# Kernel tuning notes

Hardware: AMD Instinct MI355X
Metric: run time of the kernel (lower is better)

## Reference

```python
import jax, jax.numpy as jnp
import numpy as np

N = 20000      # number of nodes
K = 32         # neighbors per node (per edge type)
D_FEAT = 128   # feature dim


def setup_inputs() -> dict:
    key = jax.random.key(0)
    k1, k2, k3 = jax.random.split(key, 3)
    feat = jax.random.normal(k1, (N, D_FEAT), dtype=jnp.float32)
    sim_idx = jax.random.randint(k2, (N, K), 0, N)
    cor_idx = jax.random.randint(k3, (N, K), 0, N)
    return {"feat": feat, "sim_idx": sim_idx, "cor_idx": cor_idx}


def _coattention(Dm, Qm):
    # Dm, Qm: [N, K, d]
    L = jnp.einsum('nkd,njd->nkj', Dm, Qm)          # [N, K, K]
    AC = jax.nn.softmax(L, axis=-1)                  # softmax over Q-neighbors
    AS = jax.nn.softmax(jnp.swapaxes(L, 1, 2), axis=-1)  # softmax over D-neighbors
    CQ = jnp.einsum('nkj,njd->nkd', AC, Qm)          # [N, K, d]
    CD = jnp.einsum('nkj,njd->nkd', AS, jnp.concatenate([Dm, CQ], axis=-1))  # [N, K, 2d]
    return jnp.concatenate([Qm, CD], axis=-1)        # [N, K, 3d]


def reference(feat, sim_idx, cor_idx):
    # mode == 'cor': D <- sim edges, Q <- cor edges (dropout=0 => identity)
    Dm = feat[sim_idx]   # [N, K, d] gather
    Qm = feat[cor_idx]   # [N, K, d] gather
    h = _coattention(Dm, Qm)                          # [N, K, 3d]
    n, k, td = h.shape
    # AvgPool1d(kernel=3, stride=3) over last dim -> [N, K, d]
    h = h.reshape(n, k, td // 3, 3).mean(axis=-1)
    h_neigh = h.mean(axis=1)                          # mean over K neighbors -> [N, d]
    return feat + h_neigh
```

## Files before the change

### kernel.cpp

```cpp
#include <hip/hip_runtime.h>

#define KN 32
#define DF 128
#define WPB 2

typedef float  f32x16 __attribute__((ext_vector_type(16)));
typedef float  f32x2  __attribute__((ext_vector_type(2)));
typedef short  s16x8  __attribute__((ext_vector_type(8)));

union ldsu { int4 i; s16x8 v; };

__device__ __forceinline__ unsigned int pk_bf16(float lo, float hi) {
    unsigned int r;
    asm("v_cvt_pk_bf16_f32 %0, %1, %2" : "=v"(r) : "v"(lo), "v"(hi));
    return r;
}

__global__ __launch_bounds__(256)
void cvt_kernel(const float* __restrict__ f, unsigned short* __restrict__ bf,
                unsigned char* __restrict__ f8, int n8) {
    const int i = blockIdx.x * blockDim.x + threadIdx.x;
    if (i >= n8) return;
    float4 x0 = ((const float4*)f)[2 * i];
    float4 x1 = ((const float4*)f)[2 * i + 1];
    int4 b;
    b.x = (int)pk_bf16(x0.x, x0.y); b.y = (int)pk_bf16(x0.z, x0.w);
    b.z = (int)pk_bf16(x1.x, x1.y); b.w = (int)pk_bf16(x1.z, x1.w);
    ((int4*)bf)[i] = b;
    int p0 = __builtin_amdgcn_cvt_pk_fp8_f32(x0.x, x0.y, 0, false);
    p0     = __builtin_amdgcn_cvt_pk_fp8_f32(x0.z, x0.w, p0, true);
    int p1 = __builtin_amdgcn_cvt_pk_fp8_f32(x1.x, x1.y, 0, false);
    p1     = __builtin_amdgcn_cvt_pk_fp8_f32(x1.z, x1.w, p1, true);
    ((int2*)f8)[i] = make_int2(p0, p1);
}

__global__ __launch_bounds__(WPB * 64, 2)
void coattn_kernel(const float* __restrict__ feat,
                   const unsigned char* __restrict__ featbf,
                   const unsigned char* __restrict__ feat8,
                   const int* __restrict__ sim_idx,
                   const int* __restrict__ cor_idx,
                   float* __restrict__ out, int nnodes) {
    __shared__ int4 Ls[WPB][2][KN][8];
    const int wv = threadIdx.x >> 6;
    const int l  = threadIdx.x & 63;
    const int c  = l & 31;
    const int h  = l >> 5;
    const int g  = l >> 3;
    const int m  = l & 7;
    const int n  = blockIdx.x * WPB + wv;
    if (n >= nnodes) return;

    const int si = sim_idx[n * KN + c];
    const int ci = cor_idx[n * KN + c];

    int4 (* const LsD)[8] = Ls[wv][0];
    int4 (* const LsQ)[8] = Ls[wv][1];

    f32x16 acc  = {0,0,0,0,0,0,0,0,0,0,0,0,0,0,0,0};
    f32x16 accT = {0,0,0,0,0,0,0,0,0,0,0,0,0,0,0,0};
    #pragma unroll
    for (int H = 0; H < 2; ++H) {
        int4 gD[4], gQ[4];
        #pragma unroll
        for (int t = 0; t < 4; ++t) {
            const unsigned rD = (unsigned)__shfl(si, 8 * t + g, 64);
            const unsigned rQ = (unsigned)__shfl(ci, 8 * t + g, 64);
            const unsigned off = (unsigned)(H * 128 + m * 16);
            gD[t] = *(const int4*)(featbf + rD * 256u + off);
            gQ[t] = *(const int4*)(featbf + rQ * 256u + off);
        }
        if (H == 1) {
            asm volatile("s_waitcnt lgkmcnt(0)" ::: "memory");
            __builtin_amdgcn_sched_barrier(0);
        }
        #pragma unroll
        for (int t = 0; t < 4; ++t) {
            LsD[8 * t + g][m ^ g] = gD[t];
            LsQ[8 * t + g][m ^ g] = gQ[t];
        }
        asm volatile("s_waitcnt lgkmcnt(0)" ::: "memory");
        __builtin_amdgcn_sched_barrier(0);
        #pragma unroll
        for (int sp = 0; sp < 4; ++sp) {
            union ldsu uD, uQ;
            uD.i = LsD[c][(sp * 2 + h) ^ (c & 7)];
            uQ.i = LsQ[c][(sp * 2 + h) ^ (c & 7)];
            acc  = __builtin_amdgcn_mfma_f32_32x32x16_bf16(uD.v, uQ.v, acc,  0, 0, 0);
            accT = __builtin_amdgcn_mfma_f32_32x32x16_bf16(uQ.v, uD.v, accT, 0, 0, 0);
        }
    }

    float mx = acc[0];
    #pragma unroll
    for (int p = 1; p < 16; ++p) mx = fmaxf(mx, acc[p]);
    mx = fmaxf(mx, __shfl_xor(mx, 32, 64));
    float z = 0.f;
    #pragma unroll
    for (int p = 0; p < 16; ++p) z += __expf(acc[p] - mx);
    z += __shfl_xor(z, 32, 64);
    const float invZ = 1.0f / z;

    float rm = accT[0];
    #pragma unroll
    for (int p = 1; p < 16; ++p) rm = fmaxf(rm, accT[p]);
    rm = fmaxf(rm, __shfl_xor(rm, 32, 64));
    float rs = 0.f;
    #pragma unroll
    for (int p = 0; p < 16; ++p) rs += __expf(accT[p] - rm);
    rs += __shfl_xor(rs, 32, 64);
    const float invR = 1.0f / rs;

    float w = 0.f;
    #pragma unroll
    for (int p = 0; p < 16; ++p) {
        const int jp = (p & 3) + 8 * (p >> 2) + 4 * h;
        w += __expf(accT[p] - __shfl(mx, jp, 64)) * __shfl(invZ, jp, 64);
    }
    w += __shfl_xor(w, 32, 64);

    const float u = w * invR;
    float v = 0.f;
    #pragma unroll
    for (int p = 0; p < 16; ++p) {
        const int kp = (p & 3) + 8 * (p >> 2) + 4 * h;
        v += __expf(acc[p] - __shfl(rm, kp, 64)) * __shfl(u, kp, 64);
    }
    v += __shfl_xor(v, 32, 64);

    float sQ[4] = {0,0,0,0}, sD[4] = {0,0,0,0}, sC[4] = {0,0,0,0};
    #pragma unroll
    for (int t = 0; t < 16; ++t) {
        const int b = h * 16 + t;
        const unsigned rD = (unsigned)__shfl(si, b, 64);
        const unsigned rQ = (unsigned)__shfl(ci, b, 64);
        const float wb = __shfl(w, b, 64);
        const float vb = __shfl(v, b, 64);
        const unsigned int da = *(const unsigned int*)(feat8 + (rD << 7) + 4u * c);
        const unsigned int dq = *(const unsigned int*)(feat8 + (rQ << 7) + 4u * c);
        f32x2 a01 = __builtin_amdgcn_cvt_pk_f32_fp8((int)da, false);
        f32x2 a23 = __builtin_amdgcn_cvt_pk_f32_fp8((int)da, true);
        f32x2 q01 = __builtin_amdgcn_cvt_pk_f32_fp8((int)dq, false);
        f32x2 q23 = __builtin_amdgcn_cvt_pk_f32_fp8((int)dq, true);
        sQ[0] += q01[0]; sQ[1] += q01[1]; sQ[2] += q23[0]; sQ[3] += q23[1];
        sD[0] = fmaf(wb, a01[0], sD[0]); sD[1] = fmaf(wb, a01[1], sD[1]);
        sD[2] = fmaf(wb, a23[0], sD[2]); sD[3] = fmaf(wb, a23[1], sD[3]);
        sC[0] = fmaf(vb, q01[0], sC[0]); sC[1] = fmaf(vb, q01[1], sC[1]);
        sC[2] = fmaf(vb, q23[0], sC[2]); sC[3] = fmaf(vb, q23[1], sC[3]);
    }
    #pragma unroll
    for (int i = 0; i < 4; ++i) {
        sQ[i] += __shfl_xor(sQ[i], 32, 64);
        sD[i] += __shfl_xor(sD[i], 32, 64);
        sC[i] += __shfl_xor(sC[i], 32, 64);
    }

    float* const S_sh = (float*)Ls[wv];
    if (h == 0) {
        *(float4*)&S_sh[0 * DF + 4 * c] = make_float4(sQ[0], sQ[1], sQ[2], sQ[3]);
        *(float4*)&S_sh[1 * DF + 4 * c] = make_float4(sD[0], sD[1], sD[2], sD[3]);
        *(float4*)&S_sh[2 * DF + 4 * c] = make_float4(sC[0], sC[1], sC[2], sC[3]);
    }
    asm volatile("s_waitcnt lgkmcnt(0)" ::: "memory");
    const float h0 = S_sh[6 * l + 0] + S_sh[6 * l + 1] + S_sh[6 * l + 2];
    const float h1 = S_sh[6 * l + 3] + S_sh[6 * l + 4] + S_sh[6 * l + 5];
    const float* fr = feat + (long)n * DF;
    const float o0 = fr[2 * l + 0] + h0 * (1.0f / 96.0f);
    const float o1 = fr[2 * l + 1] + h1 * (1.0f / 96.0f);
    *(float2*)&out[(long)n * DF + 2 * l] = make_float2(o0, o1);
}

#define RP 136
__global__ __launch_bounds__(64, 2)
void coattn_v4(const float* __restrict__ feat,
               const int* __restrict__ sim_idx,
               const int* __restrict__ cor_idx,
               float* __restrict__ out, int nnodes) {
    __shared__ unsigned char lds[2 * KN * RP];
    unsigned char* Ab8 = lds;
    unsigned char* Bb8 = lds + KN * RP;
    float* S_sh = (float*)lds;
    const int n = blockIdx.x;
    const int l = threadIdx.x;
    const int c = l & 31;
    const int h = l >> 5;
    const int si = sim_idx[n * KN + c];
    const int ci = cor_idx[n * KN + c];
    const float* Dr = feat + (long)si * DF;
    const float* Qr = feat + (long)ci * DF;
    f32x16 acc  = {0,0,0,0,0,0,0,0,0,0,0,0,0,0,0,0};
    f32x16 accT = {0,0,0,0,0,0,0,0,0,0,0,0,0,0,0,0};
    #pragma unroll
    for (int s = 0; s < 8; ++s) {
        const int d0 = s * 16 + h * 8;
        float4 a0 = *(const float4*)(Dr + d0);
        float4 a1 = *(const float4*)(Dr + d0 + 4);
        float4 b0 = *(const float4*)(Qr + d0);
        float4 b1 = *(const float4*)(Qr + d0 + 4);
        union { s16x8 v8; unsigned int u[4]; } ua, ub;
        ua.u[0] = pk_bf16(a0.x, a0.y); ua.u[1] = pk_bf16(a0.z, a0.w);
        ua.u[2] = pk_bf16(a1.x, a1.y); ua.u[3] = pk_bf16(a1.z, a1.w);
        ub.u[0] = pk_bf16(b0.x, b0.y); ub.u[1] = pk_bf16(b0.z, b0.w);
        ub.u[2] = pk_bf16(b1.x, b1.y); ub.u[3] = pk_bf16(b1.z, b1.w);
        acc  = __builtin_amdgcn_mfma_f32_32x32x16_bf16(ua.v8, ub.v8, acc,  0, 0, 0);
        accT = __builtin_amdgcn_mfma_f32_32x32x16_bf16(ub.v8, ua.v8, accT, 0, 0, 0);
        int pa0 = __builtin_amdgcn_cvt_pk_fp8_f32(a0.x, a0.y, 0, false);
        pa0     = __builtin_amdgcn_cvt_pk_fp8_f32(a0.z, a0.w, pa0, true);
        int pa1 = __builtin_amdgcn_cvt_pk_fp8_f32(a1.x, a1.y, 0, false);
        pa1     = __builtin_amdgcn_cvt_pk_fp8_f32(a1.z, a1.w, pa1, true);
        int pb0 = __builtin_amdgcn_cvt_pk_fp8_f32(b0.x, b0.y, 0, false);
        pb0     = __builtin_amdgcn_cvt_pk_fp8_f32(b0.z, b0.w, pb0, true);
        int pb1 = __builtin_amdgcn_cvt_pk_fp8_f32(b1.x, b1.y, 0, false);
        pb1     = __builtin_amdgcn_cvt_pk_fp8_f32(b1.z, b1.w, pb1, true);
        *(int2*)(Ab8 + c * RP + d0) = make_int2(pa0, pa1);
        *(int2*)(Bb8 + c * RP + d0) = make_int2(pb0, pb1);
    }
    float mx = acc[0];
    #pragma unroll
    for (int p = 1; p < 16; ++p) mx = fmaxf(mx, acc[p]);
    mx = fmaxf(mx, __shfl_xor(mx, 32, 64));
    float z = 0.f;
    #pragma unroll
    for (int p = 0; p < 16; ++p) z += __expf(acc[p] - mx);
    z += __shfl_xor(z, 32, 64);
    const float invZ = 1.0f / z;
    float rm = accT[0];
    #pragma unroll
    for (int p = 1; p < 16; ++p) rm = fmaxf(rm, accT[p]);
    rm = fmaxf(rm, __shfl_xor(rm, 32, 64));
    float rs = 0.f;
    #pragma unroll
    for (int p = 0; p < 16; ++p) rs += __expf(accT[p] - rm);
    rs += __shfl_xor(rs, 32, 64);
    const float invR = 1.0f / rs;
    float w = 0.f;
    #pragma unroll
    for (int p = 0; p < 16; ++p) {
        const int jp = (p & 3) + 8 * (p >> 2) + 4 * h;
        w += __expf(accT[p] - __shfl(mx, jp, 64)) * __shfl(invZ, jp, 64);
    }
    w += __shfl_xor(w, 32, 64);
    const float u = w * invR;
    float v = 0.f;
    #pragma unroll
    for (int p = 0; p < 16; ++p) {
        const int kp = (p & 3) + 8 * (p >> 2) + 4 * h;
        v += __expf(acc[p] - __shfl(rm, kp, 64)) * __shfl(u, kp, 64);
    }
    v += __shfl_xor(v, 32, 64);
    __syncthreads();
    float sQ[4] = {0,0,0,0}, sD[4] = {0,0,0,0}, sC[4] = {0,0,0,0};
    const unsigned char* Abase = Ab8 + h * 16 * RP + 4 * c;
    const unsigned char* Bbase = Bb8 + h * 16 * RP + 4 * c;
    #pragma unroll
    for (int t = 0; t < 16; ++t) {
        const int b = h * 16 + t;
        const float wb = __shfl(w, b, 64);
        const float vb = __shfl(v, b, 64);
        const unsigned int da = *(const unsigned int*)(Abase + t * RP);
        const unsigned int dq = *(const unsigned int*)(Bbase + t * RP);
        f32x2 a01 = __builtin_amdgcn_cvt_pk_f32_fp8((int)da, false);
        f32x2 a23 = __builtin_amdgcn_cvt_pk_f32_fp8((int)da, true);
        f32x2 q01 = __builtin_amdgcn_cvt_pk_f32_fp8((int)dq, false);
        f32x2 q23 = __builtin_amdgcn_cvt_pk_f32_fp8((int)dq, true);
        sQ[0] += q01[0]; sQ[1] += q01[1]; sQ[2] += q23[0]; sQ[3] += q23[1];
        sD[0] = fmaf(wb, a01[0], sD[0]); sD[1] = fmaf(wb, a01[1], sD[1]);
        sD[2] = fmaf(wb, a23[0], sD[2]); sD[3] = fmaf(wb, a23[1], sD[3]);
        sC[0] = fmaf(vb, q01[0], sC[0]); sC[1] = fmaf(vb, q01[1], sC[1]);
        sC[2] = fmaf(vb, q23[0], sC[2]);
        sC[3] = fmaf(vb, q23[1], sC[3]);
    }
    #pragma unroll
    for (int i = 0; i < 4; ++i) {
        sQ[i] += __shfl_xor(sQ[i], 32, 64);
        sD[i] += __shfl_xor(sD[i], 32, 64);
        sC[i] += __shfl_xor(sC[i], 32, 64);
    }
    __syncthreads();
    if (h == 0) {
        *(float4*)&S_sh[0 * DF + 4 * c] = make_float4(sQ[0], sQ[1], sQ[2], sQ[3]);
        *(float4*)&S_sh[1 * DF + 4 * c] = make_float4(sD[0], sD[1], sD[2], sD[3]);
        *(float4*)&S_sh[2 * DF + 4 * c] = make_float4(sC[0], sC[1], sC[2], sC[3]);
    }
    __syncthreads();
    const float h0 = S_sh[6 * l + 0] + S_sh[6 * l + 1] + S_sh[6 * l + 2];
    const float h1 = S_sh[6 * l + 3] + S_sh[6 * l + 4] + S_sh[6 * l + 5];
    const float* fr = feat + (long)n * DF;
    const float o0 = fr[2 * l + 0] + h0 * (1.0f / 96.0f);
    const float o1 = fr[2 * l + 1] + h1 * (1.0f / 96.0f);
    *(float2*)&out[(long)n * DF + 2 * l] = make_float2(o0, o1);
}

extern "C" void kernel_launch(void* const* d_in, const int* in_sizes, int n_in,
                              void* d_out, int out_size, void* d_ws, size_t ws_size,
                              hipStream_t stream) {
    const float* feat = (const float*)d_in[0];
    const int* sim    = (const int*)d_in[1];
    const int* cor    = (const int*)d_in[2];
    float* out        = (float*)d_out;
    const int nnodes  = in_sizes[0] / DF;
    const size_t nfeat = (size_t)nnodes * DF;
    const size_t need  = nfeat * 2 + nfeat;

    if (ws_size >= need) {
        unsigned short* featbf = (unsigned short*)d_ws;
        unsigned char*  feat8  = (unsigned char*)d_ws + nfeat * 2;
        const int n8 = (int)(nfeat / 8);
        hipLaunchKernelGGL(cvt_kernel, dim3((n8 + 255) / 256), dim3(256), 0, stream,
                           feat, featbf, feat8, n8);
        const int blocks = (nnodes + WPB - 1) / WPB;
        hipLaunchKernelGGL(coattn_kernel, dim3(blocks), dim3(WPB * 64), 0, stream,
                           feat, (const unsigned char*)featbf, feat8, sim, cor, out, nnodes);
    } else {
        hipLaunchKernelGGL(coattn_v4, dim3(nnodes), dim3(64), 0, stream,
                           feat, sim, cor, out, nnodes);
    }
}
```

Measured before the change: 62.79 us.

## Issue all bf16 and fp8 neighbor gathers upfront before MFMA and softmax

All gathers are now issued at the start of the kernel. That covers both halves of the bf16 feature rows used for the score MFMAs and the fp8 rows used in the final weighted-sum phase. Previously the second bf16 half and all the fp8 loads were issued only after earlier work had finished. Issuing them early lets their memory latency overlap with the MFMA and softmax computation. The cost is much higher register pressure (16 extra int4 values plus 32 dwords held per lane), which may lower occupancy or cause spills.

```diff
diff --git a/kernel.cpp b/kernel.cpp
--- a/kernel.cpp
+++ b/kernel.cpp
@@ -57,38 +57,60 @@
     int4 (* const LsD)[8] = Ls[wv][0];
     int4 (* const LsQ)[8] = Ls[wv][1];
 
+    int4 gD0[4], gD1[4], gQ0[4], gQ1[4];
+    #pragma unroll
+    for (int t = 0; t < 4; ++t) {
+        const unsigned rD = (unsigned)__shfl(si, 8 * t + g, 64);
+        const unsigned rQ = (unsigned)__shfl(ci, 8 * t + g, 64);
+        const unsigned off = (unsigned)(m * 16);
+        gD0[t] = *(const int4*)(featbf + rD * 256u + off);
+        gQ0[t] = *(const int4*)(featbf + rQ * 256u + off);
+        gD1[t] = *(const int4*)(featbf + rD * 256u + 128u + off);
+        gQ1[t] = *(const int4*)(featbf + rQ * 256u + 128u + off);
+    }
+
+    unsigned int da[16], dq[16];
+    #pragma unroll
+    for (int t = 0; t < 16; ++t) {
+        const unsigned rD = (unsigned)__shfl(si, h * 16 + t, 64);
+        const unsigned rQ = (unsigned)__shfl(ci, h * 16 + t, 64);
+        da[t] = *(const unsigned int*)(feat8 + (rD << 7) + 4u * c);
+        dq[t] = *(const unsigned int*)(feat8 + (rQ << 7) + 4u * c);
+    }
+
     f32x16 acc  = {0,0,0,0,0,0,0,0,0,0,0,0,0,0,0,0};
     f32x16 accT = {0,0,0,0,0,0,0,0,0,0,0,0,0,0,0,0};
     #pragma unroll
-    for (int H = 0; H < 2; ++H) {
-        int4 gD[4], gQ[4];
-        #pragma unroll
-        for (int t = 0; t < 4; ++t) {
-            const unsigned rD = (unsigned)__shfl(si, 8 * t + g, 64);
-            const unsigned rQ = (unsigned)__shfl(ci, 8 * t + g, 64);
-            const unsigned off = (unsigned)(H * 128 + m * 16);
-            gD[t] = *(const int4*)(featbf + rD * 256u + off);
-            gQ[t] = *(const int4*)(featbf + rQ * 256u + off);
-        }
-        if (H == 1) {
-            asm volatile("s_waitcnt lgkmcnt(0)" ::: "memory");
-            __builtin_amdgcn_sched_barrier(0);
-        }
-        #pragma unroll
-        for (int t = 0; t < 4; ++t) {
-            LsD[8 * t + g][m ^ g] = gD[t];
-            LsQ[8 * t + g][m ^ g] = gQ[t];
-        }
-        asm volatile("s_waitcnt lgkmcnt(0)" ::: "memory");
-        __builtin_amdgcn_sched_barrier(0);
-        #pragma unroll
-        for (int sp = 0; sp < 4; ++sp) {
-            union ldsu uD, uQ;
-            uD.i = LsD[c][(sp * 2 + h) ^ (c & 7)];
-            uQ.i = LsQ[c][(sp * 2 + h) ^ (c & 7)];
-            acc  = __builtin_amdgcn_mfma_f32_32x32x16_bf16(uD.v, uQ.v, acc,  0, 0, 0);
-            accT = __builtin_amdgcn_mfma_f32_32x32x16_bf16(uQ.v, uD.v, accT, 0, 0, 0);
-        }
+    for (int t = 0; t < 4; ++t) {
+        LsD[8 * t + g][m ^ g] = gD0[t];
+        LsQ[8 * t + g][m ^ g] = gQ0[t];
+    }
+    asm volatile("s_waitcnt lgkmcnt(0)" ::: "memory");
+    __builtin_amdgcn_sched_barrier(0);
+    #pragma unroll
+    for (int sp = 0; sp < 4; ++sp) {
+        union ldsu uD, uQ;
+        uD.i = LsD[c][(sp * 2 + h) ^ (c & 7)];
+        uQ.i = LsQ[c][(sp * 2 + h) ^ (c & 7)];
+        acc  = __builtin_amdgcn_mfma_f32_32x32x16_bf16(uD.v, uQ.v, acc,  0, 0, 0);
+        accT = __builtin_amdgcn_mfma_f32_32x32x16_bf16(uQ.v, uD.v, accT, 0, 0, 0);
+    }
+    asm volatile("s_waitcnt lgkmcnt(0)" ::: "memory");
+    __builtin_amdgcn_sched_barrier(0);
+    #pragma unroll
+    for (int t = 0; t < 4; ++t) {
+        LsD[8 * t + g][m ^ g] = gD1[t];
+        LsQ[8 * t + g][m ^ g] = gQ1[t];
+    }
+    asm volatile("s_waitcnt lgkmcnt(0)" ::: "memory");
+    __builtin_amdgcn_sched_barrier(0);
+    #pragma unroll
+    for (int sp = 0; sp < 4; ++sp) {
+        union ldsu uD, uQ;
+        uD.i = LsD[c][(sp * 2 + h) ^ (c & 7)];
+        uQ.i = LsQ[c][(sp * 2 + h) ^ (c & 7)];
+        acc  = __builtin_amdgcn_mfma_f32_32x32x16_bf16(uD.v, uQ.v, acc,  0, 0, 0);
+        accT = __builtin_amdgcn_mfma_f32_32x32x16_bf16(uQ.v, uD.v, accT, 0, 0, 0);
     }
 
     float mx = acc[0];
@@ -132,16 +154,12 @@
     #pragma unroll
     for (int t = 0; t < 16; ++t) {
         const int b = h * 16 + t;
-        const unsigned rD = (unsigned)__shfl(si, b, 64);
-        const unsigned rQ = (unsigned)__shfl(ci, b, 64);
         const float wb = __shfl(w, b, 64);
         const float vb = __shfl(v, b, 64);
-        const unsigned int da = *(const unsigned int*)(feat8 + (rD << 7) + 4u * c);
-        const unsigned int dq = *(const unsigned int*)(feat8 + (rQ << 7) + 4u * c);
-        f32x2 a01 = __builtin_amdgcn_cvt_pk_f32_fp8((int)da, false);
-        f32x2 a23 = __builtin_amdgcn_cvt_pk_f32_fp8((int)da, true);
-        f32x2 q01 = __builtin_amdgcn_cvt_pk_f32_fp8((int)dq, false);
-        f32x2 q23 = __builtin_amdgcn_cvt_pk_f32_fp8((int)dq, true);
+        f32x2 a01 = __builtin_amdgcn_cvt_pk_f32_fp8((int)da[t], false);
+        f32x2 a23 = __builtin_amdgcn_cvt_pk_f32_fp8((int)da[t], true);
+        f32x2 q01 = __builtin_amdgcn_cvt_pk_f32_fp8((int)dq[t], false);
+        f32x2 q23 = __builtin_amdgcn_cvt_pk_f32_fp8((int)dq[t], true);
         sQ[0] += q01[0]; sQ[1] += q01[1]; sQ[2] += q23[0]; sQ[3] += q23[1];
         sD[0] = fmaf(wb, a01[0], sD[0]); sD[1] = fmaf(wb, a01[1], sD[1]);
         sD[2] = fmaf(wb, a23[0], sD[2]); sD[3] = fmaf(wb, a23[1], sD[3]);
```

New measurement: 63.01 us. About the same (+0.4%).

## Load gathered bf16 rows directly into LDS via global_load_lds

Applied to the files above, without the earlier changes.

Replaces the register-staged gather (global load to VGPRs, then ds_write) with global_load_lds direct-to-LDS transfers. It uses a single LDS buffer per wave, loading D first, reading its fragments into registers, then reusing the buffer for Q. The aim is to cut LDS usage and VGPR pressure and to drop the ds_write instructions. The cost is serialization: D and Q loads are no longer issued together, and there are extra full vmcnt waits per half. The wave-uniform LDS base with per-lane swizzled global offsets must place rows correctly for the XOR layout.

```diff
diff --git a/kernel.cpp b/kernel.cpp
--- a/kernel.cpp
+++ b/kernel.cpp
@@ -14,6 +14,13 @@
     unsigned int r;
     asm("v_cvt_pk_bf16_f32 %0, %1, %2" : "=v"(r) : "v"(lo), "v"(hi));
     return r;
+}
+
+__device__ __forceinline__ void gll16(const void* g, void* l) {
+    __builtin_amdgcn_global_load_lds(
+        (const __attribute__((address_space(1))) unsigned int*)g,
+        (__attribute__((address_space(3))) unsigned int*)l,
+        16, 0, 0);
 }
 
 __global__ __launch_bounds__(256)
@@ -41,7 +48,7 @@
                    const int* __restrict__ sim_idx,
                    const int* __restrict__ cor_idx,
                    float* __restrict__ out, int nnodes) {
-    __shared__ int4 Ls[WPB][2][KN][8];
+    __shared__ int4 Ls[WPB][KN][8];
     const int wv = threadIdx.x >> 6;
     const int l  = threadIdx.x & 63;
     const int c  = l & 31;
@@ -53,42 +60,43 @@
 
     const int si = sim_idx[n * KN + c];
     const int ci = cor_idx[n * KN + c];
-
-    int4 (* const LsD)[8] = Ls[wv][0];
-    int4 (* const LsQ)[8] = Ls[wv][1];
+    const unsigned swz = (unsigned)(((m ^ g) & 7) * 16);
 
     f32x16 acc  = {0,0,0,0,0,0,0,0,0,0,0,0,0,0,0,0};
     f32x16 accT = {0,0,0,0,0,0,0,0,0,0,0,0,0,0,0,0};
     #pragma unroll
     for (int H = 0; H < 2; ++H) {
-        int4 gD[4], gQ[4];
+        const unsigned hoff = (unsigned)(H * 128) + swz;
         #pragma unroll
         for (int t = 0; t < 4; ++t) {
             const unsigned rD = (unsigned)__shfl(si, 8 * t + g, 64);
-            const unsigned rQ = (unsigned)__shfl(ci, 8 * t + g, 64);
-            const unsigned off = (unsigned)(H * 128 + m * 16);
-            gD[t] = *(const int4*)(featbf + rD * 256u + off);
-            gQ[t] = *(const int4*)(featbf + rQ * 256u + off);
+            gll16(featbf + rD * 256u + hoff, (void*)&Ls[wv][8 * t][0]);
         }
-        if (H == 1) {
-            asm volatile("s_waitcnt lgkmcnt(0)" ::: "memory");
-            __builtin_amdgcn_sched_barrier(0);
-        }
+        asm volatile("s_waitcnt vmcnt(0)" ::: "memory");
+        __builtin_amdgcn_sched_barrier(0);
+        s16x8 fD[4];
         #pragma unroll
-        for (int t = 0; t < 4; ++t) {
-            LsD[8 * t + g][m ^ g] = gD[t];
-            LsQ[8 * t + g][m ^ g] = gQ[t];
+        for (int sp = 0; sp < 4; ++sp) {
+            union ldsu u; u.i = Ls[wv][c][(sp * 2 + h) ^ (c & 7)];
+            fD[sp] = u.v;
         }
         asm volatile("s_waitcnt lgkmcnt(0)" ::: "memory");
         __builtin_amdgcn_sched_barrier(0);
         #pragma unroll
+        for (int t = 0; t < 4; ++t) {
+            const unsigned rQ = (unsigned)__shfl(ci, 8 * t + g, 64);
+            gll16(featbf + rQ * 256u + hoff, (void*)&Ls[wv][8 * t][0]);
+        }
+        asm volatile("s_waitcnt vmcnt(0)" ::: "memory");
+        __builtin_amdgcn_sched_barrier(0);
+        #pragma unroll
         for (int sp = 0; sp < 4; ++sp) {
-            union ldsu uD, uQ;
-            uD.i = LsD[c][(sp * 2 + h) ^ (c & 7)];
-            uQ.i = LsQ[c][(sp * 2 + h) ^ (c & 7)];
-            acc  = __builtin_amdgcn_mfma_f32_32x32x16_bf16(uD.v, uQ.v, acc,  0, 0, 0);
-            accT = __builtin_amdgcn_mfma_f32_32x32x16_bf16(uQ.v, uD.v, accT, 0, 0, 0);
+            union ldsu uQ; uQ.i = Ls[wv][c][(sp * 2 + h) ^ (c & 7)];
+            acc  = __builtin_amdgcn_mfma_f32_32x32x16_bf16(fD[sp], uQ.v, acc,  0, 0, 0);
+            accT = __builtin_amdgcn_mfma_f32_32x32x16_bf16(uQ.v, fD[sp], accT, 0, 0, 0);
         }
+        asm volatile("s_waitcnt lgkmcnt(0)" ::: "memory");
+        __builtin_amdgcn_sched_barrier(0);
     }
 
     float mx = acc[0];
```

Measured after the change: 61.91 us. Within noise of the previous version (-1.4%).
